# Performance work log

Hardware: AMD Instinct MI355X
Metric: run time of the kernel (lower is better)

## Reference

```python
import jax, jax.numpy as jnp
import numpy as np

B, S, D, H = 8, 1024, 1024, 16
HD = D // H


def setup_inputs() -> dict:
    key = jax.random.key(0)
    ks = jax.random.split(key, 7)
    sd = 1.0 / np.sqrt(D)
    return {
        "x": jax.random.normal(ks[0], (B, S, D), dtype=jnp.float32),
        "Wq": jax.random.normal(ks[1], (D, D), dtype=jnp.float32) * sd,
        "bq": jnp.zeros((D,), dtype=jnp.float32),
        "Wk": jax.random.normal(ks[2], (D, D), dtype=jnp.float32) * sd,
        "bk": jnp.zeros((D,), dtype=jnp.float32),
        "Wv": jax.random.normal(ks[3], (D, D), dtype=jnp.float32) * sd,
        "bv": jnp.zeros((D,), dtype=jnp.float32),
    }


def reference(x, Wq, bq, Wk, bk, Wv, bv):
    # separate Q/K/V projections (as in the source)
    q = x @ Wq + bq
    k = x @ Wk + bk
    v = x @ Wv + bv
    # [B, H, S, HD]
    q = q.reshape(B, S, H, HD).transpose(0, 2, 1, 3)
    k = k.reshape(B, S, H, HD).transpose(0, 2, 1, 3)
    v = v.reshape(B, S, H, HD).transpose(0, 2, 1, 3)
    scale = jnp.sqrt(jnp.float32(D))  # note: sqrt(embed_dim), faithful to source
    scores = jnp.einsum("bhqd,bhkd->bhqk", q, k) / scale
    attn_prob = jax.nn.softmax(scores, axis=-1)  # [B, H, S, S]
    out = jnp.einsum("bhqk,bhkd->bhqd", attn_prob, v)
    out = out.transpose(0, 2, 1, 3).reshape(B, S, D)
    return out, attn_prob
```

## Files before the change

kernel.cpp:

```cpp
#include <hip/hip_runtime.h>
#include <stdint.h>

#define B_ 8
#define S_ 1024
#define D_ 1024
#define H_ 16
#define HD_ 64
#define KPAD 72
#define VPAD 136
#define PPAD 136

typedef short bf16x8 __attribute__((ext_vector_type(8)));
typedef float f32x4 __attribute__((ext_vector_type(4)));

__device__ __forceinline__ unsigned short f2bf(float f) {
    union { float f; unsigned int u; } v; v.f = f;
    unsigned int r = v.u + 0x7FFFu + ((v.u >> 16) & 1u);
    return (unsigned short)(r >> 16);
}

__device__ __forceinline__ void xpose4(float v[4]) {
    const int ln = threadIdx.x & 3;
    float x0 = (ln & 1) ? v[0] : v[1];
    float x1 = (ln & 1) ? v[2] : v[3];
    x0 = __shfl_xor(x0, 1);
    x1 = __shfl_xor(x1, 1);
    if (ln & 1) { v[0] = x0; v[2] = x1; } else { v[1] = x0; v[3] = x1; }
    float y0 = (ln & 2) ? v[0] : v[2];
    float y1 = (ln & 2) ? v[1] : v[3];
    y0 = __shfl_xor(y0, 2);
    y1 = __shfl_xor(y1, 2);
    if (ln & 2) { v[0] = y0; v[1] = y1; } else { v[2] = y0; v[3] = y1; }
}

__global__ __launch_bounds__(256) void cast_x_kernel(const float* __restrict__ x,
                                                     unsigned short* __restrict__ xb, int n4) {
    int i = blockIdx.x * 256 + threadIdx.x;
    if (i >= n4) return;
    float4 v = ((const float4*)x)[i];
    ushort4 o;
    o.x = f2bf(v.x); o.y = f2bf(v.y); o.z = f2bf(v.z); o.w = f2bf(v.w);
    ((ushort4*)xb)[i] = o;
}

__global__ __launch_bounds__(256) void transpose_w_kernel(const float* __restrict__ Wq,
                                                          const float* __restrict__ Wk,
                                                          const float* __restrict__ Wv,
                                                          unsigned short* __restrict__ Wt) {
    __shared__ float t[32][33];
    const int z = blockIdx.z;
    const float* W = (z == 0) ? Wq : (z == 1 ? Wk : Wv);
    int bx = blockIdx.x * 32, by = blockIdx.y * 32;
    int tx = threadIdx.x, ty = threadIdx.y;
    for (int i = 0; i < 4; i++)
        t[ty + 8 * i][tx] = W[(size_t)(by + ty + 8 * i) * D_ + bx + tx];
    __syncthreads();
    unsigned short* o = Wt + (size_t)z * D_ * D_;
    for (int i = 0; i < 4; i++)
        o[(size_t)(bx + ty + 8 * i) * D_ + by + tx] = f2bf(t[tx][ty + 8 * i]);
}

__global__ __launch_bounds__(256) void qkv_gemm_kernel(const unsigned short* __restrict__ Xb,
                                                       const unsigned short* __restrict__ Wt,
                                                       const float* __restrict__ bq,
                                                       const float* __restrict__ bk,
                                                       const float* __restrict__ bv,
                                                       unsigned short* __restrict__ Yb) {
    __shared__ unsigned short Xs[128 * KPAD];
    __shared__ unsigned short Ws[128 * KPAD];

    const int which = blockIdx.y >> 3;
    const int n0 = (blockIdx.y & 7) * 128;
    const int m0 = blockIdx.x * 128;
    const int tid = threadIdx.x;
    const int wave = tid >> 6, lane = tid & 63, quad = lane >> 4, l15 = lane & 15;
    const int wm = wave >> 1, wn = wave & 1;

    const float* bias = (which == 0) ? bq : (which == 1 ? bk : bv);
    const float scale = (which == 0) ? 0.03125f : 1.0f;
    const unsigned short* Wm = Wt + (size_t)which * D_ * D_;

    f32x4 zero = {0.f, 0.f, 0.f, 0.f};
    f32x4 acc[4][4];
    for (int mt = 0; mt < 4; mt++)
        for (int nt = 0; nt < 4; nt++) acc[mt][nt] = zero;

    for (int kt = 0; kt < 16; kt++) {
        const int k0 = kt * 64;
        __syncthreads();
        for (int i = 0; i < 4; i++) {
            int c = tid + 256 * i;
            int row = c >> 3, cc = (c & 7) * 8;
            *(int4*)&Xs[row * KPAD + cc] = *(const int4*)&Xb[(size_t)(m0 + row) * D_ + k0 + cc];
            *(int4*)&Ws[row * KPAD + cc] = *(const int4*)&Wm[(size_t)(n0 + row) * D_ + k0 + cc];
        }
        __syncthreads();
        bf16x8 af[4][2];
        for (int mt = 0; mt < 4; mt++)
            for (int ks = 0; ks < 2; ks++)
                af[mt][ks] = *(const bf16x8*)&Xs[(wm * 64 + mt * 16 + l15) * KPAD + ks * 32 + quad * 8];
        for (int nt = 0; nt < 4; nt++) {
            bf16x8 b0 = *(const bf16x8*)&Ws[(wn * 64 + nt * 16 + l15) * KPAD + quad * 8];
            bf16x8 b1 = *(const bf16x8*)&Ws[(wn * 64 + nt * 16 + l15) * KPAD + 32 + quad * 8];
            for (int mt = 0; mt < 4; mt++) {
                acc[mt][nt] = __builtin_amdgcn_mfma_f32_16x16x32_bf16(af[mt][0], b0, acc[mt][nt], 0, 0, 0);
                acc[mt][nt] = __builtin_amdgcn_mfma_f32_16x16x32_bf16(af[mt][1], b1, acc[mt][nt], 0, 0, 0);
            }
        }
    }

    if (which < 2) {
        unsigned short* Y = Yb + (size_t)which * (size_t)(B_ * S_) * D_;
        for (int mt = 0; mt < 4; mt++) {
            int rbase = m0 + wm * 64 + mt * 16 + quad * 4;
            for (int nt = 0; nt < 4; nt++) {
                int colL = n0 + wn * 64 + nt * 16 + l15;
                float bcol = bias[colL];
                float p[4];
                for (int r = 0; r < 4; r++) p[r] = (acc[mt][nt][r] + bcol) * scale;
                xpose4(p);
                int row = rbase + (l15 & 3);
                int col = n0 + wn * 64 + nt * 16 + (l15 >> 2) * 4;
                ushort4 o;
                o.x = f2bf(p[0]); o.y = f2bf(p[1]); o.z = f2bf(p[2]); o.w = f2bf(p[3]);
                *(ushort4*)&Y[(size_t)row * D_ + col] = o;
            }
        }
    } else {
        unsigned short* Vt = Yb + (size_t)2 * (size_t)(B_ * S_) * D_;
        for (int mt = 0; mt < 4; mt++) {
            int m = m0 + wm * 64 + mt * 16 + quad * 4;
            int bb = m >> 10, s = m & 1023;
            for (int nt = 0; nt < 4; nt++) {
                int col = n0 + wn * 64 + nt * 16 + l15;
                float bcol = bias[col];
                ushort4 o;
                o.x = f2bf(acc[mt][nt][0] + bcol);
                o.y = f2bf(acc[mt][nt][1] + bcol);
                o.z = f2bf(acc[mt][nt][2] + bcol);
                o.w = f2bf(acc[mt][nt][3] + bcol);
                *(ushort4*)&Vt[((size_t)(bb * 16 + (col >> 6)) * 64 + (col & 63)) * S_ + s] = o;
            }
        }
    }
}

__global__ __launch_bounds__(256) void attn_kernel(const unsigned short* __restrict__ Qb,
                                                   const unsigned short* __restrict__ Kb,
                                                   const unsigned short* __restrict__ Vtg,
                                                   float* __restrict__ out,
                                                   float* __restrict__ attnp) {
    __shared__ unsigned short Ks[128 * KPAD];
    __shared__ unsigned short Vts[64 * VPAD];
    __shared__ unsigned short Ps[128 * PPAD];

    const int bh = blockIdx.y;
    const int b = bh >> 4, h = bh & 15;
    const int q0 = blockIdx.x * 128;
    const int tid = threadIdx.x;
    const int wave = tid >> 6, lane = tid & 63, quad = lane >> 4, l15 = lane & 15;

    const unsigned short* Vg = Vtg + (size_t)(b * 16 + h) * 64 * S_;

    bf16x8 qf[2][2];
    for (int mt = 0; mt < 2; mt++)
        for (int ks = 0; ks < 2; ks++)
            qf[mt][ks] = *(const bf16x8*)&Qb[(size_t)(b * S_ + q0 + wave * 32 + mt * 16 + l15) * D_ +
                                            h * HD_ + ks * 32 + quad * 8];

    float mrun[2][4], lrun[2][4];
    for (int mt = 0; mt < 2; mt++)
        for (int r = 0; r < 4; r++) { mrun[mt][r] = -1e30f; lrun[mt][r] = 0.f; }

    f32x4 zero = {0.f, 0.f, 0.f, 0.f};

    for (int kt = 0; kt < 8; kt++) {
        __syncthreads();
        for (int i = 0; i < 4; i++) {
            int c = tid + 256 * i;
            int row = c >> 3, cc = (c & 7) * 8;
            *(int4*)&Ks[row * KPAD + cc] = *(const int4*)&Kb[(size_t)(b * S_ + kt * 128 + row) * D_ + h * HD_ + cc];
        }
        __syncthreads();
        f32x4 acc[2][8];
        for (int mt = 0; mt < 2; mt++)
            for (int nt = 0; nt < 8; nt++) acc[mt][nt] = zero;
        for (int nt = 0; nt < 8; nt++) {
            bf16x8 b0 = *(const bf16x8*)&Ks[(nt * 16 + l15) * KPAD + quad * 8];
            bf16x8 b1 = *(const bf16x8*)&Ks[(nt * 16 + l15) * KPAD + 32 + quad * 8];
            for (int mt = 0; mt < 2; mt++) {
                acc[mt][nt] = __builtin_amdgcn_mfma_f32_16x16x32_bf16(qf[mt][0], b0, acc[mt][nt], 0, 0, 0);
                acc[mt][nt] = __builtin_amdgcn_mfma_f32_16x16x32_bf16(qf[mt][1], b1, acc[mt][nt], 0, 0, 0);
            }
        }
        for (int mt = 0; mt < 2; mt++) {
            for (int r = 0; r < 4; r++) {
                float tm = acc[mt][0][r];
                for (int nt = 1; nt < 8; nt++) tm = fmaxf(tm, acc[mt][nt][r]);
                for (int d = 1; d < 16; d <<= 1) tm = fmaxf(tm, __shfl_xor(tm, d));
                float mnew = fmaxf(mrun[mt][r], tm);
                float s = 0.f;
                for (int nt = 0; nt < 8; nt++) s += __expf(acc[mt][nt][r] - mnew);
                for (int d = 1; d < 16; d <<= 1) s += __shfl_xor(s, d);
                lrun[mt][r] = lrun[mt][r] * __expf(mrun[mt][r] - mnew) + s;
                mrun[mt][r] = mnew;
            }
        }
    }

    float invl[2][4];
    for (int mt = 0; mt < 2; mt++)
        for (int r = 0; r < 4; r++) invl[mt][r] = 1.0f / lrun[mt][r];

    f32x4 oacc[2][4];
    for (int mt = 0; mt < 2; mt++)
        for (int nv = 0; nv < 4; nv++) oacc[mt][nv] = zero;

    float* attn_base = attnp + (size_t)bh * S_ * S_;

    for (int kt = 0; kt < 8; kt++) {
        __syncthreads();
        for (int i = 0; i < 4; i++) {
            int c = tid + 256 * i;
            int krow = c >> 3, kcc = (c & 7) * 8;
            *(int4*)&Ks[krow * KPAD + kcc] = *(const int4*)&Kb[(size_t)(b * S_ + kt * 128 + krow) * D_ + h * HD_ + kcc];
            int vrow = c >> 4, vcc = (c & 15) * 8;
            *(int4*)&Vts[vrow * VPAD + vcc] = *(const int4*)&Vg[(size_t)vrow * S_ + kt * 128 + vcc];
        }
        __syncthreads();
        f32x4 acc[2][8];
        for (int mt = 0; mt < 2; mt++)
            for (int nt = 0; nt < 8; nt++) acc[mt][nt] = zero;
        for (int nt = 0; nt < 8; nt++) {
            bf16x8 b0 = *(const bf16x8*)&Ks[(nt * 16 + l15) * KPAD + quad * 8];
            bf16x8 b1 = *(const bf16x8*)&Ks[(nt * 16 + l15) * KPAD + 32 + quad * 8];
            for (int mt = 0; mt < 2; mt++) {
                acc[mt][nt] = __builtin_amdgcn_mfma_f32_16x16x32_bf16(qf[mt][0], b0, acc[mt][nt], 0, 0, 0);
                acc[mt][nt] = __builtin_amdgcn_mfma_f32_16x16x32_bf16(qf[mt][1], b1, acc[mt][nt], 0, 0, 0);
            }
        }
        for (int mt = 0; mt < 2; mt++) {
            for (int nt = 0; nt < 8; nt++) {
                float p[4];
                for (int r = 0; r < 4; r++)
                    p[r] = __expf(acc[mt][nt][r] - mrun[mt][r]) * invl[mt][r];
                xpose4(p);
                int rl = wave * 32 + mt * 16 + quad * 4 + (l15 & 3);
                int cl = nt * 16 + (l15 >> 2) * 4;
                float4 f4; f4.x = p[0]; f4.y = p[1]; f4.z = p[2]; f4.w = p[3];
                *(float4*)&attn_base[(size_t)(q0 + rl) * S_ + kt * 128 + cl] = f4;
                unsigned int lo = ((unsigned int)f2bf(p[1]) << 16) | f2bf(p[0]);
                unsigned int hi = ((unsigned int)f2bf(p[3]) << 16) | f2bf(p[2]);
                *(uint2*)&Ps[rl * PPAD + cl] = make_uint2(lo, hi);
            }
        }
        __syncthreads();
        for (int kc = 0; kc < 4; kc++) {
            bf16x8 af[2];
            for (int mt = 0; mt < 2; mt++)
                af[mt] = *(const bf16x8*)&Ps[(wave * 32 + mt * 16 + l15) * PPAD + kc * 32 + quad * 8];
            for (int nv = 0; nv < 4; nv++) {
                bf16x8 bfv = *(const bf16x8*)&Vts[(nv * 16 + l15) * VPAD + kc * 32 + quad * 8];
                for (int mt = 0; mt < 2; mt++)
                    oacc[mt][nv] = __builtin_amdgcn_mfma_f32_16x16x32_bf16(af[mt], bfv, oacc[mt][nv], 0, 0, 0);
            }
        }
    }

    for (int mt = 0; mt < 2; mt++) {
        for (int nv = 0; nv < 4; nv++) {
            float o[4];
            for (int r = 0; r < 4; r++) o[r] = oacc[mt][nv][r];
            xpose4(o);
            int row = q0 + wave * 32 + mt * 16 + quad * 4 + (l15 & 3);
            int col = h * HD_ + nv * 16 + (l15 >> 2) * 4;
            float4 f4; f4.x = o[0]; f4.y = o[1]; f4.z = o[2]; f4.w = o[3];
            *(float4*)&out[(size_t)(b * S_ + row) * D_ + col] = f4;
        }
    }
}

extern "C" void kernel_launch(void* const* d_in, const int* in_sizes, int n_in,
                              void* d_out, int out_size, void* d_ws, size_t ws_size,
                              hipStream_t stream) {
    const float* x  = (const float*)d_in[0];
    const float* Wq = (const float*)d_in[1];
    const float* bq = (const float*)d_in[2];
    const float* Wk = (const float*)d_in[3];
    const float* bk = (const float*)d_in[4];
    const float* Wv = (const float*)d_in[5];
    const float* bv = (const float*)d_in[6];
    float* out = (float*)d_out;
    float* attnp = out + (size_t)B_ * S_ * D_;

    unsigned short* Xb = (unsigned short*)d_ws;
    unsigned short* Wt = Xb + (size_t)B_ * S_ * D_;
    unsigned short* Yb = Wt + (size_t)3 * D_ * D_;
    unsigned short* Qb = Yb;
    unsigned short* Kb = Yb + (size_t)B_ * S_ * D_;
    unsigned short* Vtg = Kb + (size_t)B_ * S_ * D_;

    int n4 = B_ * S_ * D_ / 4;
    cast_x_kernel<<<(n4 + 255) / 256, 256, 0, stream>>>(x, Xb, n4);
    transpose_w_kernel<<<dim3(32, 32, 3), dim3(32, 8), 0, stream>>>(Wq, Wk, Wv, Wt);
    qkv_gemm_kernel<<<dim3(64, 24), 256, 0, stream>>>(Xb, Wt, bq, bk, bv, Yb);
    attn_kernel<<<dim3(8, 128), 256, 0, stream>>>(Qb, Kb, Vtg, out, attnp);
}
```

Measured before the change: 837.7 us.

## Read K/V fragments directly from global memory and swap attention grid axes

```diff
diff --git a/kernel.cpp b/kernel.cpp
--- a/kernel.cpp
+++ b/kernel.cpp
@@ -7,7 +7,6 @@
 #define H_ 16
 #define HD_ 64
 #define KPAD 72
-#define VPAD 136
 #define PPAD 136
 
 typedef short bf16x8 __attribute__((ext_vector_type(8)));
@@ -150,17 +149,16 @@
                                                    const unsigned short* __restrict__ Vtg,
                                                    float* __restrict__ out,
                                                    float* __restrict__ attnp) {
-    __shared__ unsigned short Ks[128 * KPAD];
-    __shared__ unsigned short Vts[64 * VPAD];
     __shared__ unsigned short Ps[128 * PPAD];
 
-    const int bh = blockIdx.y;
+    const int bh = blockIdx.x;
     const int b = bh >> 4, h = bh & 15;
-    const int q0 = blockIdx.x * 128;
+    const int q0 = blockIdx.y * 128;
     const int tid = threadIdx.x;
     const int wave = tid >> 6, lane = tid & 63, quad = lane >> 4, l15 = lane & 15;
 
-    const unsigned short* Vg = Vtg + (size_t)(b * 16 + h) * 64 * S_;
+    const unsigned short* Kh = Kb + (size_t)(b * S_) * D_ + h * HD_;
+    const unsigned short* Vg = Vtg + (size_t)bh * HD_ * S_;
 
     bf16x8 qf[2][2];
     for (int mt = 0; mt < 2; mt++)
@@ -175,19 +173,13 @@
     f32x4 zero = {0.f, 0.f, 0.f, 0.f};
 
     for (int kt = 0; kt < 8; kt++) {
-        __syncthreads();
-        for (int i = 0; i < 4; i++) {
-            int c = tid + 256 * i;
-            int row = c >> 3, cc = (c & 7) * 8;
-            *(int4*)&Ks[row * KPAD + cc] = *(const int4*)&Kb[(size_t)(b * S_ + kt * 128 + row) * D_ + h * HD_ + cc];
-        }
-        __syncthreads();
         f32x4 acc[2][8];
         for (int mt = 0; mt < 2; mt++)
             for (int nt = 0; nt < 8; nt++) acc[mt][nt] = zero;
         for (int nt = 0; nt < 8; nt++) {
-            bf16x8 b0 = *(const bf16x8*)&Ks[(nt * 16 + l15) * KPAD + quad * 8];
-            bf16x8 b1 = *(const bf16x8*)&Ks[(nt * 16 + l15) * KPAD + 32 + quad * 8];
+            const unsigned short* krow = &Kh[(size_t)(kt * 128 + nt * 16 + l15) * D_ + quad * 8];
+            bf16x8 b0 = *(const bf16x8*)krow;
+            bf16x8 b1 = *(const bf16x8*)(krow + 32);
             for (int mt = 0; mt < 2; mt++) {
                 acc[mt][nt] = __builtin_amdgcn_mfma_f32_16x16x32_bf16(qf[mt][0], b0, acc[mt][nt], 0, 0, 0);
                 acc[mt][nt] = __builtin_amdgcn_mfma_f32_16x16x32_bf16(qf[mt][1], b1, acc[mt][nt], 0, 0, 0);
@@ -219,26 +211,19 @@
     float* attn_base = attnp + (size_t)bh * S_ * S_;
 
     for (int kt = 0; kt < 8; kt++) {
-        __syncthreads();
-        for (int i = 0; i < 4; i++) {
-            int c = tid + 256 * i;
-            int krow = c >> 3, kcc = (c & 7) * 8;
-            *(int4*)&Ks[krow * KPAD + kcc] = *(const int4*)&Kb[(size_t)(b * S_ + kt * 128 + krow) * D_ + h * HD_ + kcc];
-            int vrow = c >> 4, vcc = (c & 15) * 8;
-            *(int4*)&Vts[vrow * VPAD + vcc] = *(const int4*)&Vg[(size_t)vrow * S_ + kt * 128 + vcc];
-        }
-        __syncthreads();
         f32x4 acc[2][8];
         for (int mt = 0; mt < 2; mt++)
             for (int nt = 0; nt < 8; nt++) acc[mt][nt] = zero;
         for (int nt = 0; nt < 8; nt++) {
-            bf16x8 b0 = *(const bf16x8*)&Ks[(nt * 16 + l15) * KPAD + quad * 8];
-            bf16x8 b1 = *(const bf16x8*)&Ks[(nt * 16 + l15) * KPAD + 32 + quad * 8];
+            const unsigned short* krow = &Kh[(size_t)(kt * 128 + nt * 16 + l15) * D_ + quad * 8];
+            bf16x8 b0 = *(const bf16x8*)krow;
+            bf16x8 b1 = *(const bf16x8*)(krow + 32);
             for (int mt = 0; mt < 2; mt++) {
                 acc[mt][nt] = __builtin_amdgcn_mfma_f32_16x16x32_bf16(qf[mt][0], b0, acc[mt][nt], 0, 0, 0);
                 acc[mt][nt] = __builtin_amdgcn_mfma_f32_16x16x32_bf16(qf[mt][1], b1, acc[mt][nt], 0, 0, 0);
             }
         }
+        __syncthreads();
         for (int mt = 0; mt < 2; mt++) {
             for (int nt = 0; nt < 8; nt++) {
                 float p[4];
@@ -260,7 +245,7 @@
             for (int mt = 0; mt < 2; mt++)
                 af[mt] = *(const bf16x8*)&Ps[(wave * 32 + mt * 16 + l15) * PPAD + kc * 32 + quad * 8];
             for (int nv = 0; nv < 4; nv++) {
-                bf16x8 bfv = *(const bf16x8*)&Vts[(nv * 16 + l15) * VPAD + kc * 32 + quad * 8];
+                bf16x8 bfv = *(const bf16x8*)&Vg[(size_t)(nv * 16 + l15) * S_ + kt * 128 + kc * 32 + quad * 8];
                 for (int mt = 0; mt < 2; mt++)
                     oacc[mt][nv] = __builtin_amdgcn_mfma_f32_16x16x32_bf16(af[mt], bfv, oacc[mt][nv], 0, 0, 0);
             }
@@ -304,5 +289,5 @@
     cast_x_kernel<<<(n4 + 255) / 256, 256, 0, stream>>>(x, Xb, n4);
     transpose_w_kernel<<<dim3(32, 32, 3), dim3(32, 8), 0, stream>>>(Wq, Wk, Wv, Wt);
     qkv_gemm_kernel<<<dim3(64, 24), 256, 0, stream>>>(Xb, Wt, bq, bk, bv, Yb);
-    attn_kernel<<<dim3(8, 128), 256, 0, stream>>>(Qb, Kb, Vtg, out, attnp);
-}
+    attn_kernel<<<dim3(128, 8), 256, 0, stream>>>(Qb, Kb, Vtg, out, attnp);
+}
```

After: 948.1 us. +13.2%, slower.

## Prefetch GEMM and K tiles into registers, read V from global, reorder attention grid

Applied to the files above, without the earlier changes.

```diff
diff --git a/kernel.cpp b/kernel.cpp
--- a/kernel.cpp
+++ b/kernel.cpp
@@ -7,7 +7,6 @@
 #define H_ 16
 #define HD_ 64
 #define KPAD 72
-#define VPAD 136
 #define PPAD 136
 
 typedef short bf16x8 __attribute__((ext_vector_type(8)));
@@ -85,20 +84,37 @@
     for (int mt = 0; mt < 4; mt++)
         for (int nt = 0; nt < 4; nt++) acc[mt][nt] = zero;
 
+    int4 xreg[4], wreg[4];
+    for (int i = 0; i < 4; i++) {
+        int c = tid + 256 * i;
+        int row = c >> 3, cc = (c & 7) * 8;
+        xreg[i] = *(const int4*)&Xb[(size_t)(m0 + row) * D_ + cc];
+        wreg[i] = *(const int4*)&Wm[(size_t)(n0 + row) * D_ + cc];
+    }
+
     for (int kt = 0; kt < 16; kt++) {
-        const int k0 = kt * 64;
         __syncthreads();
         for (int i = 0; i < 4; i++) {
             int c = tid + 256 * i;
             int row = c >> 3, cc = (c & 7) * 8;
-            *(int4*)&Xs[row * KPAD + cc] = *(const int4*)&Xb[(size_t)(m0 + row) * D_ + k0 + cc];
-            *(int4*)&Ws[row * KPAD + cc] = *(const int4*)&Wm[(size_t)(n0 + row) * D_ + k0 + cc];
-        }
-        __syncthreads();
+            *(int4*)&Xs[row * KPAD + cc] = xreg[i];
+            *(int4*)&Ws[row * KPAD + cc] = wreg[i];
+        }
+        __syncthreads();
+        if (kt < 15) {
+            const int k1 = (kt + 1) * 64;
+            for (int i = 0; i < 4; i++) {
+                int c = tid + 256 * i;
+                int row = c >> 3, cc = (c & 7) * 8;
+                xreg[i] = *(const int4*)&Xb[(size_t)(m0 + row) * D_ + k1 + cc];
+                wreg[i] = *(const int4*)&Wm[(size_t)(n0 + row) * D_ + k1 + cc];
+            }
+        }
         bf16x8 af[4][2];
         for (int mt = 0; mt < 4; mt++)
             for (int ks = 0; ks < 2; ks++)
                 af[mt][ks] = *(const bf16x8*)&Xs[(wm * 64 + mt * 16 + l15) * KPAD + ks * 32 + quad * 8];
+        __builtin_amdgcn_s_setprio(1);
         for (int nt = 0; nt < 4; nt++) {
             bf16x8 b0 = *(const bf16x8*)&Ws[(wn * 64 + nt * 16 + l15) * KPAD + quad * 8];
             bf16x8 b1 = *(const bf16x8*)&Ws[(wn * 64 + nt * 16 + l15) * KPAD + 32 + quad * 8];
@@ -107,6 +123,7 @@
                 acc[mt][nt] = __builtin_amdgcn_mfma_f32_16x16x32_bf16(af[mt][1], b1, acc[mt][nt], 0, 0, 0);
             }
         }
+        __builtin_amdgcn_s_setprio(0);
     }
 
     if (which < 2) {
@@ -151,16 +168,16 @@
                                                    float* __restrict__ out,
                                                    float* __restrict__ attnp) {
     __shared__ unsigned short Ks[128 * KPAD];
-    __shared__ unsigned short Vts[64 * VPAD];
     __shared__ unsigned short Ps[128 * PPAD];
 
-    const int bh = blockIdx.y;
+    const int bh = blockIdx.x;
     const int b = bh >> 4, h = bh & 15;
-    const int q0 = blockIdx.x * 128;
+    const int q0 = blockIdx.y * 128;
     const int tid = threadIdx.x;
     const int wave = tid >> 6, lane = tid & 63, quad = lane >> 4, l15 = lane & 15;
 
-    const unsigned short* Vg = Vtg + (size_t)(b * 16 + h) * 64 * S_;
+    const unsigned short* Kh = Kb + (size_t)(b * S_) * D_ + h * HD_;
+    const unsigned short* Vg = Vtg + (size_t)bh * HD_ * S_;
 
     bf16x8 qf[2][2];
     for (int mt = 0; mt < 2; mt++)
@@ -174,17 +191,29 @@
 
     f32x4 zero = {0.f, 0.f, 0.f, 0.f};
 
+    int4 kreg[4];
+    for (int i = 0; i < 4; i++) {
+        int c = tid + 256 * i;
+        kreg[i] = *(const int4*)&Kh[(size_t)(c >> 3) * D_ + (c & 7) * 8];
+    }
+
     for (int kt = 0; kt < 8; kt++) {
         __syncthreads();
         for (int i = 0; i < 4; i++) {
             int c = tid + 256 * i;
-            int row = c >> 3, cc = (c & 7) * 8;
-            *(int4*)&Ks[row * KPAD + cc] = *(const int4*)&Kb[(size_t)(b * S_ + kt * 128 + row) * D_ + h * HD_ + cc];
-        }
-        __syncthreads();
+            *(int4*)&Ks[(c >> 3) * KPAD + (c & 7) * 8] = kreg[i];
+        }
+        __syncthreads();
+        if (kt < 7) {
+            for (int i = 0; i < 4; i++) {
+                int c = tid + 256 * i;
+                kreg[i] = *(const int4*)&Kh[(size_t)((kt + 1) * 128 + (c >> 3)) * D_ + (c & 7) * 8];
+            }
+        }
         f32x4 acc[2][8];
         for (int mt = 0; mt < 2; mt++)
             for (int nt = 0; nt < 8; nt++) acc[mt][nt] = zero;
+        __builtin_amdgcn_s_setprio(1);
         for (int nt = 0; nt < 8; nt++) {
             bf16x8 b0 = *(const bf16x8*)&Ks[(nt * 16 + l15) * KPAD + quad * 8];
             bf16x8 b1 = *(const bf16x8*)&Ks[(nt * 16 + l15) * KPAD + 32 + quad * 8];
@@ -193,6 +222,7 @@
                 acc[mt][nt] = __builtin_amdgcn_mfma_f32_16x16x32_bf16(qf[mt][1], b1, acc[mt][nt], 0, 0, 0);
             }
         }
+        __builtin_amdgcn_s_setprio(0);
         for (int mt = 0; mt < 2; mt++) {
             for (int r = 0; r < 4; r++) {
                 float tm = acc[mt][0][r];
@@ -218,19 +248,28 @@
 
     float* attn_base = attnp + (size_t)bh * S_ * S_;
 
+    for (int i = 0; i < 4; i++) {
+        int c = tid + 256 * i;
+        kreg[i] = *(const int4*)&Kh[(size_t)(c >> 3) * D_ + (c & 7) * 8];
+    }
+
     for (int kt = 0; kt < 8; kt++) {
         __syncthreads();
         for (int i = 0; i < 4; i++) {
             int c = tid + 256 * i;
-            int krow = c >> 3, kcc = (c & 7) * 8;
-            *(int4*)&Ks[krow * KPAD + kcc] = *(const int4*)&Kb[(size_t)(b * S_ + kt * 128 + krow) * D_ + h * HD_ + kcc];
-            int vrow = c >> 4, vcc = (c & 15) * 8;
-            *(int4*)&Vts[vrow * VPAD + vcc] = *(const int4*)&Vg[(size_t)vrow * S_ + kt * 128 + vcc];
-        }
-        __syncthreads();
+            *(int4*)&Ks[(c >> 3) * KPAD + (c & 7) * 8] = kreg[i];
+        }
+        __syncthreads();
+        if (kt < 7) {
+            for (int i = 0; i < 4; i++) {
+                int c = tid + 256 * i;
+                kreg[i] = *(const int4*)&Kh[(size_t)((kt + 1) * 128 + (c >> 3)) * D_ + (c & 7) * 8];
+            }
+        }
         f32x4 acc[2][8];
         for (int mt = 0; mt < 2; mt++)
             for (int nt = 0; nt < 8; nt++) acc[mt][nt] = zero;
+        __builtin_amdgcn_s_setprio(1);
         for (int nt = 0; nt < 8; nt++) {
             bf16x8 b0 = *(const bf16x8*)&Ks[(nt * 16 + l15) * KPAD + quad * 8];
             bf16x8 b1 = *(const bf16x8*)&Ks[(nt * 16 + l15) * KPAD + 32 + quad * 8];
@@ -239,6 +278,7 @@
                 acc[mt][nt] = __builtin_amdgcn_mfma_f32_16x16x32_bf16(qf[mt][1], b1, acc[mt][nt], 0, 0, 0);
             }
         }
+        __builtin_amdgcn_s_setprio(0);
         for (int mt = 0; mt < 2; mt++) {
             for (int nt = 0; nt < 8; nt++) {
                 float p[4];
@@ -254,17 +294,18 @@
                 *(uint2*)&Ps[rl * PPAD + cl] = make_uint2(lo, hi);
             }
         }
-        __syncthreads();
+        __builtin_amdgcn_s_setprio(1);
         for (int kc = 0; kc < 4; kc++) {
             bf16x8 af[2];
             for (int mt = 0; mt < 2; mt++)
                 af[mt] = *(const bf16x8*)&Ps[(wave * 32 + mt * 16 + l15) * PPAD + kc * 32 + quad * 8];
             for (int nv = 0; nv < 4; nv++) {
-                bf16x8 bfv = *(const bf16x8*)&Vts[(nv * 16 + l15) * VPAD + kc * 32 + quad * 8];
+                bf16x8 bfv = *(const bf16x8*)&Vg[(size_t)(nv * 16 + l15) * S_ + kt * 128 + kc * 32 + quad * 8];
                 for (int mt = 0; mt < 2; mt++)
                     oacc[mt][nv] = __builtin_amdgcn_mfma_f32_16x16x32_bf16(af[mt], bfv, oacc[mt][nv], 0, 0, 0);
             }
         }
+        __builtin_amdgcn_s_setprio(0);
     }
 
     for (int mt = 0; mt < 2; mt++) {
@@ -304,5 +345,5 @@
     cast_x_kernel<<<(n4 + 255) / 256, 256, 0, stream>>>(x, Xb, n4);
     transpose_w_kernel<<<dim3(32, 32, 3), dim3(32, 8), 0, stream>>>(Wq, Wk, Wv, Wt);
     qkv_gemm_kernel<<<dim3(64, 24), 256, 0, stream>>>(Xb, Wt, bq, bk, bv, Yb);
-    attn_kernel<<<dim3(8, 128), 256, 0, stream>>>(Qb, Kb, Vtg, out, attnp);
-}
+    attn_kernel<<<dim3(128, 8), 256, 0, stream>>>(Qb, Kb, Vtg, out, attnp);
+}
```

After: 1.011 ms. 20.7% more time.
